# Kernel tuning notes

Measured on AMD Instinct MI355X. Metric: run time of the kernel, lower is better.

The kernel has to match this reference:

```python
import jax, jax.numpy as jnp
import numpy as np

N, C, T, V = 16, 256, 256, 64   # batch, node_channel_in, time, total_nodes
SC, SV = 3, 64                  # node_channel_out, num_seeds
NEW_NODES, C_OUT = 64, 3
IN_DIM = C * V + SC * SV        # 16576


def setup_inputs() -> dict:
    key = jax.random.key(0)
    k1, k2, k3, k4 = jax.random.split(key, 4)
    x = jax.random.normal(k1, (N, C, T, V), dtype=jnp.float32)
    seeds = jax.random.normal(k2, (N, T, SC, SV), dtype=jnp.float32)
    # Stacked weights of the `new_nodes` independent Linear(IN_DIM, C_OUT) layers
    W = jax.random.normal(k3, (NEW_NODES, C_OUT, IN_DIM), dtype=jnp.float32) * 0.02
    b = jax.random.normal(k4, (NEW_NODES, C_OUT), dtype=jnp.float32) * 0.02
    return {"x": x, "seeds": seeds, "W": W, "b": b}


def reference(x, seeds, W, b):
    n, c, t, v = x.shape
    # (n,c,t,v) -> (n,t,c*v)
    xm = jnp.transpose(x, (0, 2, 1, 3)).reshape(n, t, c * v)
    sm = seeds.reshape(n, t, -1)                 # (n,t,sc*sv)
    mix = jnp.concatenate([xm, sm], axis=2)      # (n,t,IN_DIM)
    # Fused horizontal GEMM over all new_nodes projections, then stacked on dim 3:
    # out[n,t,c_out,j] = sum_k mix[n,t,k] * W[j,c_out,k] + b[j,c_out]
    out = jnp.einsum('ntk,jck->ntcj', mix, W) + b.T[None, None]
    return out  # (n, t, node_channel_out, new_nodes)
```

## Files before the change

### kernel.cpp

```cpp
#include <hip/hip_runtime.h>
#include <hip/hip_bf16.h>

typedef unsigned short u16;
typedef unsigned int   u32;
typedef __attribute__((ext_vector_type(8))) short bf16x8;
typedef __attribute__((ext_vector_type(4))) float f32x4;

#define NB    16
#define CIN   256
#define TDIM  256
#define VDIM  64
#define PCOL  192
#define NCHX  256
#define NCH   259
#define MTOT  4096
#define CHUNK_U16 12288
#define WT_BYTES ((size_t)NCH * CHUNK_U16 * 2)

__device__ __forceinline__ u16 f2bf(float f) {
  u32 u = __builtin_bit_cast(u32, f);
  u32 r = u + 0x7fffu + ((u >> 16) & 1u);
  return (u16)(r >> 16);
}
__device__ __forceinline__ u32 pk2(float a, float b) {
  return (u32)f2bf(a) | ((u32)f2bf(b) << 16);
}

__global__ void prep_w(const float* __restrict__ W, u16* __restrict__ Wt) {
  int u  = blockIdx.x * 256 + threadIdx.x;
  int q  = u & 7;
  int p  = (u >> 3) % PCOL;
  int ch = u / (PCOL * 8);
  int j = p & 63, co = p >> 6;
  const float* src = W + (size_t)(j * 3 + co) * 16576 + ch * 64 + q * 8;
  float4 fa = *(const float4*)src;
  float4 fb = *(const float4*)(src + 4);
  uint4 v;
  v.x = pk2(fa.x, fa.y); v.y = pk2(fa.z, fa.w);
  v.z = pk2(fb.x, fb.y); v.w = pk2(fb.z, fb.w);
  int wid = p / 48, within = p % 48;
  int nt = within >> 4, lr = within & 15;
  int ks = q >> 2,      lq = q & 3;
  int r = nt * 2 + ks, lane = lq * 16 + lr;
  ((uint4*)Wt)[(size_t)ch * 1536 + wid * 384 + r * 64 + lane] = v;
}

__global__ __launch_bounds__(256, 2)
void gemm_bf16(const float* __restrict__ x, const float* __restrict__ seeds,
               const u16* __restrict__ Wt, float* __restrict__ dst,
               const float* __restrict__ bias, int S) {
  __shared__ __align__(16) u16 ldsA[2][4096];
  const int tid  = threadIdx.x;
  const int lane = tid & 63;
  const int wid  = tid >> 6;
  const int bid  = blockIdx.x;
  int mblk, ksp;
  if (S == 8) { ksp = bid & 7;  mblk = bid >> 3; }
  else        { mblk = bid & 63; ksp = bid >> 6; }
  const int n  = mblk >> 2;
  const int t0 = (mblk & 3) << 6;
  const int c0 = (NCH * ksp) / S;
  const int c1 = (NCH * (ksp + 1)) / S;

  const int q0 = tid & 7;
  const int m0 = tid >> 3;
  const int lr = lane & 15, lq = lane >> 4;

  f32x4 acc[4][3] = {};

  struct ASet { float4 r0a, r0b, r1a, r1b; };
  struct BSet { uint4 r0, r1, r2, r3, r4, r5; };
  ASet AX, AY;
  BSet BX, BY;

  const char* bbase = (const char*)Wt + wid * 6144 + lane * 16;

  auto Bi = [&](int ch, BSet& s) {
    const uint4* g = (const uint4*)(bbase + (size_t)ch * 24576);
    s.r0 = g[0];   s.r1 = g[64];  s.r2 = g[128];
    s.r3 = g[192]; s.r4 = g[256]; s.r5 = g[320];
  };
  auto Ai = [&](int ch, ASet& s) {
    const float *a0, *a1;
    if (ch < NCHX) {
      a0 = x + (((size_t)n * CIN + ch) * TDIM + (t0 + m0)) * VDIM + q0 * 8;
      a1 = a0 + (size_t)32 * VDIM;
    } else {
      a0 = seeds + ((size_t)n * TDIM + (t0 + m0)) * 192 + (ch - NCHX) * 64 + q0 * 8;
      a1 = a0 + (size_t)32 * 192;
    }
    s.r0a = *(const float4*)a0; s.r0b = *(const float4*)(a0 + 4);
    s.r1a = *(const float4*)a1; s.r1b = *(const float4*)(a1 + 4);
  };
  auto CONV = [&](const ASet& s, int buf) {
    uint4 v;
    v.x = pk2(s.r0a.x, s.r0a.y); v.y = pk2(s.r0a.z, s.r0a.w);
    v.z = pk2(s.r0b.x, s.r0b.y); v.w = pk2(s.r0b.z, s.r0b.w);
    ((uint4*)&ldsA[buf][0])[m0 * 8 + (q0 ^ (m0 & 7))] = v;
    int m1 = m0 + 32;
    v.x = pk2(s.r1a.x, s.r1a.y); v.y = pk2(s.r1a.z, s.r1a.w);
    v.z = pk2(s.r1b.x, s.r1b.y); v.w = pk2(s.r1b.z, s.r1b.w);
    ((uint4*)&ldsA[buf][0])[m1 * 8 + (q0 ^ (m1 & 7))] = v;
  };

  auto COMPUTE = [&](int buf, const BSet& B) {
    const u16* L = &ldsA[buf][0];
    #pragma unroll
    for (int ks = 0; ks < 2; ++ks) {
      const int q = ks * 4 + lq;
      bf16x8 af[4];
      #pragma unroll
      for (int mt = 0; mt < 4; ++mt) {
        int m = mt * 16 + lr;
        af[mt] = *(const bf16x8*)(L + (m * 8 + (q ^ (m & 7))) * 8);
      }
      bf16x8 b0 = __builtin_bit_cast(bf16x8, ks ? B.r1 : B.r0);
      bf16x8 b1 = __builtin_bit_cast(bf16x8, ks ? B.r3 : B.r2);
      bf16x8 b2 = __builtin_bit_cast(bf16x8, ks ? B.r5 : B.r4);
      #pragma unroll
      for (int mt = 0; mt < 4; ++mt) {
        acc[mt][0] = __builtin_amdgcn_mfma_f32_16x16x32_bf16(af[mt], b0, acc[mt][0], 0, 0, 0);
        acc[mt][1] = __builtin_amdgcn_mfma_f32_16x16x32_bf16(af[mt], b1, acc[mt][1], 0, 0, 0);
        acc[mt][2] = __builtin_amdgcn_mfma_f32_16x16x32_bf16(af[mt], b2, acc[mt][2], 0, 0, 0);
      }
    }
  };

  Bi(c0, BX);
  Ai(c0, AX);
  if (c0 + 1 < c1) { Bi(c0 + 1, BY); Ai(c0 + 1, AY); }
  __builtin_amdgcn_sched_barrier(0);
  CONV(AX, 0);
  asm volatile("s_waitcnt lgkmcnt(0)" ::: "memory");
  __builtin_amdgcn_sched_barrier(0);
  __builtin_amdgcn_s_barrier();
  __builtin_amdgcn_sched_barrier(0);

#define PHASE(PAR, AP, AN, BC)                                                \
  {                                                                           \
    const bool hasN  = (ch + 1 < c1);                                         \
    const bool hasNN = (ch + 2 < c1);                                         \
    if (hasNN) Ai(ch + 2, AN);                                                \
    __builtin_amdgcn_sched_barrier(0);                                        \
    COMPUTE(PAR, BC);                                                         \
    __builtin_amdgcn_sched_barrier(0);                                        \
    if (hasNN) Bi(ch + 2, BC);                  \
    if (!hasN) break;                                                         \
    CONV(AP, (PAR) ^ 1);                   \
    asm volatile("s_waitcnt lgkmcnt(0)" ::: "memory");                        \
    __builtin_amdgcn_sched_barrier(0);                                        \
    __builtin_amdgcn_s_barrier();                                             \
    __builtin_amdgcn_sched_barrier(0);                                        \
  }

  int ch = c0;
  while (true) {
    PHASE(0, AY, AX, BX)
    ++ch;
    PHASE(1, AX, AY, BY)
    ++ch;
  }
#undef PHASE

  float* dbase = dst + (size_t)ksp * MTOT * PCOL;
  #pragma unroll
  for (int mt = 0; mt < 4; ++mt)
    #pragma unroll
    for (int nt = 0; nt < 3; ++nt) {
      int col = wid * 48 + nt * 16 + lr;
      float bv = bias ? bias[(col & 63) * 3 + (col >> 6)] : 0.f;
      #pragma unroll
      for (int r = 0; r < 4; ++r) {
        int row = mblk * 64 + mt * 16 + lq * 4 + r;
        dbase[(size_t)row * PCOL + col] = acc[mt][nt][r] + bv;
      }
    }
}

__global__ void reduce_k(const float* __restrict__ part, const float* __restrict__ b,
                         float* __restrict__ out, int S) {
  int i4 = (blockIdx.x * 256 + threadIdx.x) * 4;
  float4 a = *(const float4*)&part[i4];
  for (int s = 1; s < S; ++s) {
    const float4 v = *(const float4*)&part[(size_t)s * (MTOT * PCOL) + i4];
    a.x += v.x; a.y += v.y; a.z += v.z; a.w += v.w;
  }
  int p0 = i4 % PCOL;
  a.x += b[((p0 + 0) & 63) * 3 + ((p0 + 0) >> 6)];
  a.y += b[((p0 + 1) & 63) * 3 + ((p0 + 1) >> 6)];
  a.z += b[((p0 + 2) & 63) * 3 + ((p0 + 2) >> 6)];
  a.w += b[((p0 + 3) & 63) * 3 + ((p0 + 3) >> 6)];
  *(float4*)&out[i4] = a;
}

__global__ void fallback_k(const float* __restrict__ x, const float* __restrict__ seeds,
                           const float* __restrict__ W, const float* __restrict__ b,
                           float* __restrict__ out) {
  __shared__ float mk[512];
  int m = blockIdx.x, n = m >> 8, t = m & 255, p = threadIdx.x;
  float acc = 0.f;
  for (int k0 = 0; k0 < 16576; k0 += 512) {
    int kn = min(512, 16576 - k0);
    __syncthreads();
    for (int i = threadIdx.x; i < kn; i += 256) {
      int k = k0 + i;
      mk[i] = (k < 16384)
                ? x[(((size_t)n * 256 + (k >> 6)) * 256 + t) * 64 + (k & 63)]
                : seeds[((size_t)n * 256 + t) * 192 + (k - 16384)];
    }
    __syncthreads();
    if (p < PCOL) {
      const float* wr = W + (size_t)((p & 63) * 3 + (p >> 6)) * 16576 + k0;
      for (int i = 0; i < kn; ++i) acc += mk[i] * wr[i];
    }
  }
  if (p < PCOL) out[(size_t)m * PCOL + p] = acc + b[(p & 63) * 3 + (p >> 6)];
}

extern "C" void kernel_launch(void* const* d_in, const int* in_sizes, int n_in,
                              void* d_out, int out_size, void* d_ws, size_t ws_size,
                              hipStream_t stream) {
  (void)in_sizes; (void)n_in; (void)out_size;
  const float* x     = (const float*)d_in[0];
  const float* seeds = (const float*)d_in[1];
  const float* W     = (const float*)d_in[2];
  const float* b     = (const float*)d_in[3];
  float* out = (float*)d_out;

  if (ws_size < WT_BYTES) {
    fallback_k<<<dim3(MTOT), dim3(256), 0, stream>>>(x, seeds, W, b, out);
    return;
  }
  u16* Wt = (u16*)d_ws;
  int S = 8;
  while (S > 1 && WT_BYTES + (size_t)S * MTOT * PCOL * 4 > ws_size) S >>= 1;
  if (WT_BYTES + (size_t)S * MTOT * PCOL * 4 > ws_size) S = 1;

  prep_w<<<dim3((NCH * PCOL * 8) / 256), dim3(256), 0, stream>>>(W, Wt);
  if (S == 1) {
    gemm_bf16<<<dim3(64), dim3(256), 0, stream>>>(x, seeds, Wt, out, b, 1);
  } else {
    float* part = (float*)((char*)d_ws + WT_BYTES);
    gemm_bf16<<<dim3(64 * S), dim3(256), 0, stream>>>(x, seeds, Wt, part, nullptr, S);
    reduce_k<<<dim3(MTOT * PCOL / 4 / 256), dim3(256), 0, stream>>>(part, b, out, S);
  }
}
```

Baseline: 80.71 us.

## Process two K-chunks per pipeline stage to halve barriers

Restructures the double-buffered main loop so each stage loads, converts and computes two 64-wide K chunks instead of one. LDS buffers double to hold both chunks, and B fragments for the pair are kept in a single 12-register array. This halves the workgroup barriers and LDS waits per K step. In exchange it adds register pressure and reduces B prefetch depth: B for the next pair is now loaded after compute, with no longer a full stage of lookahead. That may expose global latency or lower occupancy under launch_bounds(256,2).

```diff
diff --git a/kernel.cpp b/kernel.cpp
--- a/kernel.cpp
+++ b/kernel.cpp
@@ -49,7 +49,7 @@
 void gemm_bf16(const float* __restrict__ x, const float* __restrict__ seeds,
                const u16* __restrict__ Wt, float* __restrict__ dst,
                const float* __restrict__ bias, int S) {
-  __shared__ __align__(16) u16 ldsA[2][4096];
+  __shared__ __align__(16) u16 ldsA[2][8192];
   const int tid  = threadIdx.x;
   const int lane = tid & 63;
   const int wid  = tid >> 6;
@@ -68,31 +68,40 @@
 
   f32x4 acc[4][3] = {};
 
-  struct ASet { float4 r0a, r0b, r1a, r1b; };
-  struct BSet { uint4 r0, r1, r2, r3, r4, r5; };
+  struct ASet { float4 r0a, r0b, r1a, r1b, r2a, r2b, r3a, r3b; };
   ASet AX, AY;
-  BSet BX, BY;
+  uint4 Breg[12];
 
   const char* bbase = (const char*)Wt + wid * 6144 + lane * 16;
 
-  auto Bi = [&](int ch, BSet& s) {
-    const uint4* g = (const uint4*)(bbase + (size_t)ch * 24576);
-    s.r0 = g[0];   s.r1 = g[64];  s.r2 = g[128];
-    s.r3 = g[192]; s.r4 = g[256]; s.r5 = g[320];
-  };
-  auto Ai = [&](int ch, ASet& s) {
-    const float *a0, *a1;
-    if (ch < NCHX) {
-      a0 = x + (((size_t)n * CIN + ch) * TDIM + (t0 + m0)) * VDIM + q0 * 8;
-      a1 = a0 + (size_t)32 * VDIM;
-    } else {
-      a0 = seeds + ((size_t)n * TDIM + (t0 + m0)) * 192 + (ch - NCHX) * 64 + q0 * 8;
-      a1 = a0 + (size_t)32 * 192;
-    }
+  auto arow = [&](int ch, int mrow) -> const float* {
+    if (ch < NCHX)
+      return x + (((size_t)n * CIN + ch) * TDIM + (t0 + mrow)) * VDIM + q0 * 8;
+    return seeds + ((size_t)n * TDIM + (t0 + mrow)) * 192 + (ch - NCHX) * 64 + q0 * 8;
+  };
+  auto Ai = [&](int cc, ASet& s) {
+    const float* a0 = arow(cc, m0);
+    const float* a1 = arow(cc, m0 + 32);
     s.r0a = *(const float4*)a0; s.r0b = *(const float4*)(a0 + 4);
     s.r1a = *(const float4*)a1; s.r1b = *(const float4*)(a1 + 4);
-  };
-  auto CONV = [&](const ASet& s, int buf) {
+    if (cc + 1 < c1) {
+      const float* b0 = arow(cc + 1, m0);
+      const float* b1 = arow(cc + 1, m0 + 32);
+      s.r2a = *(const float4*)b0; s.r2b = *(const float4*)(b0 + 4);
+      s.r3a = *(const float4*)b1; s.r3b = *(const float4*)(b1 + 4);
+    }
+  };
+  auto Bi = [&](int cc) {
+    const uint4* g0 = (const uint4*)(bbase + (size_t)cc * 24576);
+    Breg[0] = g0[0];   Breg[1] = g0[64];  Breg[2] = g0[128];
+    Breg[3] = g0[192]; Breg[4] = g0[256]; Breg[5] = g0[320];
+    if (cc + 1 < c1) {
+      const uint4* g1 = (const uint4*)(bbase + (size_t)(cc + 1) * 24576);
+      Breg[6]  = g1[0];   Breg[7]  = g1[64];  Breg[8]  = g1[128];
+      Breg[9]  = g1[192]; Breg[10] = g1[256]; Breg[11] = g1[320];
+    }
+  };
+  auto CONV = [&](const ASet& s, int buf, int cc) {
     uint4 v;
     v.x = pk2(s.r0a.x, s.r0a.y); v.y = pk2(s.r0a.z, s.r0a.w);
     v.z = pk2(s.r0b.x, s.r0b.y); v.w = pk2(s.r0b.z, s.r0b.w);
@@ -101,64 +110,76 @@
     v.x = pk2(s.r1a.x, s.r1a.y); v.y = pk2(s.r1a.z, s.r1a.w);
     v.z = pk2(s.r1b.x, s.r1b.y); v.w = pk2(s.r1b.z, s.r1b.w);
     ((uint4*)&ldsA[buf][0])[m1 * 8 + (q0 ^ (m1 & 7))] = v;
-  };
-
-  auto COMPUTE = [&](int buf, const BSet& B) {
-    const u16* L = &ldsA[buf][0];
+    if (cc + 1 < c1) {
+      v.x = pk2(s.r2a.x, s.r2a.y); v.y = pk2(s.r2a.z, s.r2a.w);
+      v.z = pk2(s.r2b.x, s.r2b.y); v.w = pk2(s.r2b.z, s.r2b.w);
+      ((uint4*)&ldsA[buf][4096])[m0 * 8 + (q0 ^ (m0 & 7))] = v;
+      v.x = pk2(s.r3a.x, s.r3a.y); v.y = pk2(s.r3a.z, s.r3a.w);
+      v.z = pk2(s.r3b.x, s.r3b.y); v.w = pk2(s.r3b.z, s.r3b.w);
+      ((uint4*)&ldsA[buf][4096])[m1 * 8 + (q0 ^ (m1 & 7))] = v;
+    }
+  };
+
+  auto COMPUTE = [&](int buf, bool hasSub1) {
     #pragma unroll
-    for (int ks = 0; ks < 2; ++ks) {
-      const int q = ks * 4 + lq;
-      bf16x8 af[4];
+    for (int sub = 0; sub < 2; ++sub) {
+      if (sub == 1 && !hasSub1) break;
+      const u16* L = &ldsA[buf][sub * 4096];
       #pragma unroll
-      for (int mt = 0; mt < 4; ++mt) {
-        int m = mt * 16 + lr;
-        af[mt] = *(const bf16x8*)(L + (m * 8 + (q ^ (m & 7))) * 8);
+      for (int ks = 0; ks < 2; ++ks) {
+        const int q = ks * 4 + lq;
+        bf16x8 af[4];
+        #pragma unroll
+        for (int mt = 0; mt < 4; ++mt) {
+          int m = mt * 16 + lr;
+          af[mt] = *(const bf16x8*)(L + (m * 8 + (q ^ (m & 7))) * 8);
+        }
+        bf16x8 b0 = __builtin_bit_cast(bf16x8, Breg[sub * 6 + 0 + ks]);
+        bf16x8 b1 = __builtin_bit_cast(bf16x8, Breg[sub * 6 + 2 + ks]);
+        bf16x8 b2 = __builtin_bit_cast(bf16x8, Breg[sub * 6 + 4 + ks]);
+        #pragma unroll
+        for (int mt = 0; mt < 4; ++mt) {
+          acc[mt][0] = __builtin_amdgcn_mfma_f32_16x16x32_bf16(af[mt], b0, acc[mt][0], 0, 0, 0);
+          acc[mt][1] = __builtin_amdgcn_mfma_f32_16x16x32_bf16(af[mt], b1, acc[mt][1], 0, 0, 0);
+          acc[mt][2] = __builtin_amdgcn_mfma_f32_16x16x32_bf16(af[mt], b2, acc[mt][2], 0, 0, 0);
+        }
       }
-      bf16x8 b0 = __builtin_bit_cast(bf16x8, ks ? B.r1 : B.r0);
-      bf16x8 b1 = __builtin_bit_cast(bf16x8, ks ? B.r3 : B.r2);
-      bf16x8 b2 = __builtin_bit_cast(bf16x8, ks ? B.r5 : B.r4);
-      #pragma unroll
-      for (int mt = 0; mt < 4; ++mt) {
-        acc[mt][0] = __builtin_amdgcn_mfma_f32_16x16x32_bf16(af[mt], b0, acc[mt][0], 0, 0, 0);
-        acc[mt][1] = __builtin_amdgcn_mfma_f32_16x16x32_bf16(af[mt], b1, acc[mt][1], 0, 0, 0);
-        acc[mt][2] = __builtin_amdgcn_mfma_f32_16x16x32_bf16(af[mt], b2, acc[mt][2], 0, 0, 0);
-      }
-    }
-  };
-
-  Bi(c0, BX);
+    }
+  };
+
+  Bi(c0);
   Ai(c0, AX);
-  if (c0 + 1 < c1) { Bi(c0 + 1, BY); Ai(c0 + 1, AY); }
+  if (c0 + 2 < c1) Ai(c0 + 2, AY);
   __builtin_amdgcn_sched_barrier(0);
-  CONV(AX, 0);
+  CONV(AX, 0, c0);
   asm volatile("s_waitcnt lgkmcnt(0)" ::: "memory");
   __builtin_amdgcn_sched_barrier(0);
   __builtin_amdgcn_s_barrier();
   __builtin_amdgcn_sched_barrier(0);
 
-#define PHASE(PAR, AP, AN, BC)                                                \
+#define PHASE(PAR, AP, AN)                                                    \
   {                                                                           \
-    const bool hasN  = (ch + 1 < c1);                                         \
-    const bool hasNN = (ch + 2 < c1);                                         \
-    if (hasNN) Ai(ch + 2, AN);                                                \
-    __builtin_amdgcn_sched_barrier(0);                                        \
-    COMPUTE(PAR, BC);                                                         \
-    __builtin_amdgcn_sched_barrier(0);                                        \
-    if (hasNN) Bi(ch + 2, BC);                  \
+    const bool hasN  = (cc + 2 < c1);                                         \
+    const bool hasNN = (cc + 4 < c1);                                         \
+    if (hasNN) Ai(cc + 4, AN);                                                \
+    __builtin_amdgcn_sched_barrier(0);                                        \
+    COMPUTE(PAR, cc + 1 < c1);                                                \
+    __builtin_amdgcn_sched_barrier(0);                                        \
+    if (hasN) Bi(cc + 2);                     \
     if (!hasN) break;                                                         \
-    CONV(AP, (PAR) ^ 1);                   \
+    CONV(AP, (PAR) ^ 1, cc + 2);           \
     asm volatile("s_waitcnt lgkmcnt(0)" ::: "memory");                        \
     __builtin_amdgcn_sched_barrier(0);                                        \
     __builtin_amdgcn_s_barrier();                                             \
     __builtin_amdgcn_sched_barrier(0);                                        \
   }
 
-  int ch = c0;
+  int cc = c0;
   while (true) {
-    PHASE(0, AY, AX, BX)
-    ++ch;
-    PHASE(1, AX, AY, BY)
-    ++ch;
+    PHASE(0, AY, AX)
+    cc += 2;
+    PHASE(1, AX, AY)
+    cc += 2;
   }
 #undef PHASE
 
```

Result: faster. 78.11 us (-3.2%).
